# Optimization experiments

Measured on AMD Instinct MI355X. Metric: run time of the kernel, lower is better.

The kernel has to match this reference:

```python
import jax, jax.numpy as jnp
import numpy as np

CAPS = 16          # num_capsules
DIM = 16           # capsule_dim
NUM_ROUTING = 3
L2_EPS = 1e-12     # tf.nn.l2_normalize epsilon


def setup_inputs() -> dict:
    key = jax.random.key(0)
    k1, k2 = jax.random.split(key)
    inputs = jax.random.normal(k1, (16, 64, 64, 128), dtype=jnp.float32)
    # Conv2D kernel, HWIO layout, fan-in scaled like glorot-ish init
    kernel = jax.random.normal(k2, (3, 3, 128, CAPS * DIM), dtype=jnp.float32) * 0.03
    bias = jnp.zeros((CAPS * DIM,), dtype=jnp.float32)
    return {"inputs": inputs, "kernel": kernel, "bias": bias}


def reference(inputs, kernel, bias):
    # Conv2D(caps*dim, 3x3, padding='same', activation='relu'), channels_last
    x = jax.lax.conv_general_dilated(
        inputs, kernel, window_strides=(1, 1), padding="SAME",
        dimension_numbers=("NHWC", "HWIO", "NHWC"))
    x = jax.nn.relu(x + bias)
    B, H, W, _ = x.shape
    x = x.reshape(B, H * W, CAPS, DIM)            # (B, N, C, D)
    b = jnp.zeros((B, H * W, CAPS), dtype=x.dtype)
    v = None
    for _ in range(NUM_ROUTING):
        c = jax.nn.softmax(b, axis=-1)             # over capsules
        s = jnp.einsum("bnc,bncd->bcd", c, x)      # weighted sum over spatial
        # tf.nn.l2_normalize along last axis
        v = s * jax.lax.rsqrt(jnp.maximum(jnp.sum(s * s, axis=-1, keepdims=True), L2_EPS))
        b = b + jnp.einsum("bncd,bcd->bnc", x, v)  # agreement update
    # tile v over spatial dims: (B,1,1,C*D) -> (B,H,W,C*D)
    out = jnp.broadcast_to(v.reshape(B, 1, 1, CAPS * DIM), (B, H, W, CAPS * DIM))
    return out
```

## Files before the change

### kernel.cpp

```cpp
#include <hip/hip_runtime.h>
#include <hip/hip_bf16.h>

typedef unsigned short u16;
typedef unsigned int   u32;

typedef __bf16 bf16x8 __attribute__((ext_vector_type(8)));
typedef float  f32x4  __attribute__((ext_vector_type(4)));

#define GLDS(gp, lp) __builtin_amdgcn_global_load_lds( \
    (const __attribute__((address_space(1))) void*)(gp), \
    (__attribute__((address_space(3))) void*)(lp), 16, 0, 0)

__device__ __forceinline__ u16 f2b(float f) {
    __hip_bfloat16 h = __float2bfloat16(f);
    u16 u; __builtin_memcpy(&u, &h, 2); return u;
}
__device__ __forceinline__ float blo(u32 u) { return __uint_as_float(u << 16); }
__device__ __forceinline__ float bhi(u32 u) { return __uint_as_float(u & 0xffff0000u); }

__global__ void k_prep(const float* __restrict__ in, const float* __restrict__ wk,
                       u16* __restrict__ pad, u16* __restrict__ BF,
                       float* __restrict__ stats) {
    int bx = blockIdx.x, tid = threadIdx.x;
    if (bx < 4356) {
        int idx = bx * 256 + tid;
        int e0  = idx * 8;
        int ch  = e0 & 127;
        int rest = e0 >> 7;
        int pw = rest % 66;
        int r2 = rest / 66;
        int ph = r2 % 66;
        int b  = r2 / 66;
        u16 ov[8];
        if (ph >= 1 && ph <= 64 && pw >= 1 && pw <= 64) {
            const float* src = in + (((b * 64 + (ph - 1)) * 64 + (pw - 1)) * 128 + ch);
            const float4* s4 = (const float4*)src;
            float4 f0 = s4[0], f1 = s4[1];
            ov[0]=f2b(f0.x); ov[1]=f2b(f0.y); ov[2]=f2b(f0.z); ov[3]=f2b(f0.w);
            ov[4]=f2b(f1.x); ov[5]=f2b(f1.y); ov[6]=f2b(f1.z); ov[7]=f2b(f1.w);
        } else {
            #pragma unroll
            for (int j = 0; j < 8; ++j) ov[j] = 0;
        }
        uint4 w; __builtin_memcpy(&w, ov, 16);
        *(uint4*)(pad + e0) = w;
    } else if (bx < 5508) {
        int t = (bx - 4356) * 256 + tid;
        int j  = t & 7;
        int n  = (t >> 3) & 255;
        int q  = (t >> 11) & 3;
        int kk = (t >> 13) & 3;
        int p  = t >> 15;
        BF[t] = f2b(wk[(p * 128 + kk * 32 + q * 8 + j) * 256 + n]);
    } else {
        stats[(bx - 5508) * 256 + tid] = 0.f;
    }
}

__launch_bounds__(512, 2)
__global__ void k_conv(const u16* __restrict__ Ap, const u16* __restrict__ BF,
                       const float* __restrict__ bias,
                       u16* __restrict__ X, float* __restrict__ s0) {
    __shared__ u16 ldsA[25344];
    const int t = threadIdx.x;
    const int lane = t & 63, wid = t >> 6;
    const int q = lane >> 4, l15 = lane & 15;
    const int bb = blockIdx.x >> 4;
    const int rg = blockIdx.x & 15;
    const int rg4 = rg << 2;
    const int wm0 = (wid >> 2) << 7;
    const int wn0 = (wid & 3) << 6;
    const int rowb = wm0 >> 6;

#define STAGE(S) { \
    const int sb0 = wid * 396; \
    _Pragma("unroll") for (int i = 0; i < 6; ++i) { \
        int slot = sb0 + i * 64 + lane; \
        int pr = slot / 528; int rem = slot - pr * 528; \
        int wp = rem >> 3, cs = rem & 7; \
        int gc = (S) * 8 + (cs ^ (wp & 7)); \
        const u16* g = Ap + ((((bb * 66 + rg4 + pr) * 66 + wp) << 7) + (gc << 3)); \
        GLDS(g, (char*)ldsA + (sb0 + i * 64) * 16); \
    } \
    { int slot = sb0 + 384 + lane; \
      if (lane < 12) { \
        int pr = slot / 528; int rem = slot - pr * 528; \
        int wp = rem >> 3, cs = rem & 7; \
        int gc = (S) * 8 + (cs ^ (wp & 7)); \
        const u16* g = Ap + ((((bb * 66 + rg4 + pr) * 66 + wp) << 7) + (gc << 3)); \
        GLDS(g, (char*)ldsA + (sb0 + 384) * 16); \
      } } }

#define LOADB(B, P, S) { \
    _Pragma("unroll") for (int kk = 0; kk < 2; ++kk) \
    _Pragma("unroll") for (int ni = 0; ni < 4; ++ni) \
        B[kk * 4 + ni] = *(const bf16x8*)(BFl + (P) * 32768 + \
                                          ((S) * 2 + kk) * 8192 + ni * 128); }

#define COMPP(B, DH, DW) { \
    _Pragma("unroll") for (int kk = 0; kk < 2; ++kk) { \
        bf16x8 af[8]; \
        _Pragma("unroll") for (int mi = 0; mi < 8; ++mi) { \
            int wp = ((mi & 3) << 4) + l15 + (DW); \
            int pr = rowb + (mi >> 2) + (DH); \
            int cc = (kk << 2) + q; \
            af[mi] = *(const bf16x8*)((const char*)ldsA + \
                ((pr * 528 + (wp << 3) + (cc ^ (wp & 7))) << 4)); \
        } \
        _Pragma("unroll") for (int mi = 0; mi < 8; ++mi) \
        _Pragma("unroll") for (int ni = 0; ni < 4; ++ni) \
            acc[mi][ni] = __builtin_amdgcn_mfma_f32_16x16x32_bf16( \
                af[mi], B[kk * 4 + ni], acc[mi][ni], 0, 0, 0); } }

    const u16* BFl = BF + (q * 2048 + (wn0 + l15) * 8);

    f32x4 zero = {0.f, 0.f, 0.f, 0.f};
    f32x4 acc[8][4];
    #pragma unroll
    for (int mi = 0; mi < 8; ++mi)
        #pragma unroll
        for (int ni = 0; ni < 4; ++ni) acc[mi][ni] = zero;

    bf16x8 B0[8], B1[8];

    STAGE(0);
    __syncthreads();
    LOADB(B0, 0, 0);
    LOADB(B1, 1, 0); COMPP(B0, 0, 0);
    LOADB(B0, 2, 0); COMPP(B1, 0, 1);
    LOADB(B1, 3, 0); COMPP(B0, 0, 2);
    LOADB(B0, 4, 0); COMPP(B1, 1, 0);
    LOADB(B1, 5, 0); COMPP(B0, 1, 1);
    LOADB(B0, 6, 0); COMPP(B1, 1, 2);
    LOADB(B1, 7, 0); COMPP(B0, 2, 0);
    LOADB(B0, 8, 0); COMPP(B1, 2, 1);
    COMPP(B0, 2, 2);
    __syncthreads();

    STAGE(1);
    __syncthreads();
    LOADB(B0, 0, 1);
    LOADB(B1, 1, 1); COMPP(B0, 0, 0);
    LOADB(B0, 2, 1); COMPP(B1, 0, 1);
    LOADB(B1, 3, 1); COMPP(B0, 0, 2);
    LOADB(B0, 4, 1); COMPP(B1, 1, 0);
    LOADB(B1, 5, 1); COMPP(B0, 1, 1);
    LOADB(B0, 6, 1); COMPP(B1, 1, 2);
    LOADB(B1, 7, 1); COMPP(B0, 2, 0);
    LOADB(B0, 8, 1); COMPP(B1, 2, 1);
    COMPP(B0, 2, 2);

    float bv[4];
    #pragma unroll
    for (int ni = 0; ni < 4; ++ni) bv[ni] = bias[wn0 + ni * 16 + l15];
    float colsum[4] = {0.f, 0.f, 0.f, 0.f};
    u16* xrow = X + (((bb << 12) + (rg << 8) + wm0 + q * 4) * 256) + wn0 + l15;
    #pragma unroll
    for (int mi = 0; mi < 8; ++mi) {
        #pragma unroll
        for (int rr = 0; rr < 4; ++rr) {
            u16* xp = xrow + (mi * 16 + rr) * 256;
            #pragma unroll
            for (int ni = 0; ni < 4; ++ni) {
                float v = acc[mi][ni][rr] + bv[ni];
                v = v > 0.f ? v : 0.f;
                xp[ni * 16] = f2b(v);
                colsum[ni] += v;
            }
        }
    }
    #pragma unroll
    for (int ni = 0; ni < 4; ++ni) {
        float c = colsum[ni];
        c += __shfl_xor(c, 16);
        c += __shfl_xor(c, 32);
        if (lane < 16) atomicAdd(&s0[bb * 256 + wn0 + ni * 16 + l15], c);
    }
#undef STAGE
#undef LOADB
#undef COMPP
}

__global__ void k_pass(const u16* __restrict__ X, const float* __restrict__ Sa,
                       const float* __restrict__ Sb, float* __restrict__ Sout,
                       int use2) {
    __shared__ float v1s[256], v2s[256];
    __shared__ float red[4096];
    int t = threadIdx.x, b = blockIdx.y, chunk = blockIdx.x;
    {
        float sa = Sa[b * 256 + t];
        float ss = sa * sa;
        #pragma unroll
        for (int off = 1; off < 16; off <<= 1) ss += __shfl_xor(ss, off);
        ss = ss < 1e-12f ? 1e-12f : ss;
        v1s[t] = sa / sqrtf(ss);
        if (use2) {
            float sb = Sb[b * 256 + t];
            float s2 = sb * sb;
            #pragma unroll
            for (int off = 1; off < 16; off <<= 1) s2 += __shfl_xor(s2, off);
            s2 = s2 < 1e-12f ? 1e-12f : s2;
            v2s[t] = sb / sqrtf(s2);
        } else {
            v2s[t] = 0.f;
        }
    }
    __syncthreads();
    int c = t & 15, nl = t >> 4;
    float acc[16];
    #pragma unroll
    for (int d = 0; d < 16; ++d) acc[d] = 0.f;

    for (int r = 0; r < 8; ++r) {
        int n = chunk * 128 + r * 16 + nl;
        const u16* xp = X + ((b << 12) + n) * 256 + c * 16;
        uint4 a0 = ((const uint4*)xp)[0];
        uint4 a1 = ((const uint4*)xp)[1];
        u32 us[8] = {a0.x, a0.y, a0.z, a0.w, a1.x, a1.y, a1.z, a1.w};
        float xf[16];
        #pragma unroll
        for (int j = 0; j < 8; ++j) { xf[2*j] = blo(us[j]); xf[2*j+1] = bhi(us[j]); }
        float d1 = 0.f, d2 = 0.f;
        #pragma unroll
        for (int d = 0; d < 16; ++d) {
            d1 += xf[d] * v1s[c * 16 + d];
            d2 += xf[d] * v2s[c * 16 + d];
        }
        float bvv = use2 ? (d1 + d2) : d1;
        float mx = bvv;
        #pragma unroll
        for (int off = 1; off < 16; off <<= 1) {
            float o = __shfl_xor(mx, off);
            mx = mx > o ? mx : o;
        }
        float e = expf(bvv - mx);
        float sm = e;
        #pragma unroll
        for (int off = 1; off < 16; off <<= 1) sm += __shfl_xor(sm, off);
        float w = e / sm;
        #pragma unroll
        for (int d = 0; d < 16; ++d) acc[d] += w * xf[d];
    }
    #pragma unroll
    for (int d = 0; d < 16; ++d) red[t * 16 + d] = acc[d];
    __syncthreads();
    int c2 = t >> 4, d2i = t & 15;
    float tot = 0.f;
    #pragma unroll
    for (int n2 = 0; n2 < 16; ++n2) tot += red[(n2 * 16 + c2) * 16 + d2i];
    atomicAdd(&Sout[b * 256 + c2 * 16 + d2i], tot);
}

__global__ void k_bcast(const float* __restrict__ S, float* __restrict__ Out) {
    __shared__ float4 vls[64];
    int t = threadIdx.x, bx = blockIdx.x, b = blockIdx.y;
    float s = S[b * 256 + t];
    float ss = s * s;
    #pragma unroll
    for (int off = 1; off < 16; off <<= 1) ss += __shfl_xor(ss, off);
    ss = ss < 1e-12f ? 1e-12f : ss;
    ((float*)vls)[t] = s / sqrtf(ss);
    __syncthreads();
    float4* o = (float4*)Out + (long)b * 262144 + bx * 8192;
    #pragma unroll
    for (int j = 0; j < 32; ++j) {
        int idx = j * 256 + t;
        o[idx] = vls[idx & 63];
    }
}

extern "C" void kernel_launch(void* const* d_in, const int* in_sizes, int n_in,
                              void* d_out, int out_size, void* d_ws, size_t ws_size,
                              hipStream_t stream) {
    const float* in   = (const float*)d_in[0];
    const float* wk   = (const float*)d_in[1];
    const float* bias = (const float*)d_in[2];
    float* out = (float*)d_out;
    char* ws = (char*)d_ws;

    const size_t OFF_PAD = 0;
    const size_t OFF_BF  = 17842176;
    const size_t OFF_X   = 18432000;
    const size_t OFF_ST  = 51986432;
    const size_t NEEDED  = OFF_ST + 3 * 16384;
    if (ws_size < NEEDED) return;

    u16* pad = (u16*)(ws + OFF_PAD);
    u16* BF  = (u16*)(ws + OFF_BF);
    u16* X   = (u16*)(ws + OFF_X);
    float* s0 = (float*)(ws + OFF_ST);
    float* s2 = s0 + 4096;
    float* s3 = s2 + 4096;

    k_prep <<<5556, 256, 0, stream>>>(in, wk, pad, BF, s0);
    k_conv <<<256, 512, 0, stream>>>(pad, BF, bias, X, s0);
    k_pass <<<dim3(32, 16), 256, 0, stream>>>(X, s0, s0, s2, 0);
    k_pass <<<dim3(32, 16), 256, 0, stream>>>(X, s0, s2, s3, 1);
    k_bcast<<<dim3(32, 16), 256, 0, stream>>>(s3, out);
}
```

Measured before the change: 183.6 us.

## Shrink conv tiles to one output row per block and split routing passes finer

```diff
diff --git a/kernel.cpp b/kernel.cpp
--- a/kernel.cpp
+++ b/kernel.cpp
@@ -57,38 +57,37 @@
     }
 }
 
-__launch_bounds__(512, 2)
+__launch_bounds__(256, 2)
 __global__ void k_conv(const u16* __restrict__ Ap, const u16* __restrict__ BF,
                        const float* __restrict__ bias,
                        u16* __restrict__ X, float* __restrict__ s0) {
-    __shared__ u16 ldsA[25344];
+    __shared__ u16 ldsA[12672];
     const int t = threadIdx.x;
     const int lane = t & 63, wid = t >> 6;
     const int q = lane >> 4, l15 = lane & 15;
-    const int bb = blockIdx.x >> 4;
-    const int rg = blockIdx.x & 15;
-    const int rg4 = rg << 2;
-    const int wm0 = (wid >> 2) << 7;
-    const int wn0 = (wid & 3) << 6;
-    const int rowb = wm0 >> 6;
+    const int bb = blockIdx.x >> 6;
+    const int h  = blockIdx.x & 63;
+    const int wn0 = wid << 6;
 
 #define STAGE(S) { \
     const int sb0 = wid * 396; \
     _Pragma("unroll") for (int i = 0; i < 6; ++i) { \
-        int slot = sb0 + i * 64 + lane; \
+        int sb = sb0 + i * 64; \
+        int slot = sb + lane; \
         int pr = slot / 528; int rem = slot - pr * 528; \
         int wp = rem >> 3, cs = rem & 7; \
         int gc = (S) * 8 + (cs ^ (wp & 7)); \
-        const u16* g = Ap + ((((bb * 66 + rg4 + pr) * 66 + wp) << 7) + (gc << 3)); \
-        GLDS(g, (char*)ldsA + (sb0 + i * 64) * 16); \
+        const u16* g = Ap + ((((bb * 66 + h + pr) * 66 + wp) << 7) + (gc << 3)); \
+        GLDS(g, (char*)ldsA + sb * 16); \
     } \
-    { int slot = sb0 + 384 + lane; \
+    { int sb = sb0 + 384; \
       if (lane < 12) { \
+        int slot = sb + lane; \
         int pr = slot / 528; int rem = slot - pr * 528; \
         int wp = rem >> 3, cs = rem & 7; \
         int gc = (S) * 8 + (cs ^ (wp & 7)); \
-        const u16* g = Ap + ((((bb * 66 + rg4 + pr) * 66 + wp) << 7) + (gc << 3)); \
-        GLDS(g, (char*)ldsA + (sb0 + 384) * 16); \
+        const u16* g = Ap + ((((bb * 66 + h + pr) * 66 + wp) << 7) + (gc << 3)); \
+        GLDS(g, (char*)ldsA + sb * 16); \
       } } }
 
 #define LOADB(B, P, S) { \
@@ -99,15 +98,14 @@
 
 #define COMPP(B, DH, DW) { \
     _Pragma("unroll") for (int kk = 0; kk < 2; ++kk) { \
-        bf16x8 af[8]; \
-        _Pragma("unroll") for (int mi = 0; mi < 8; ++mi) { \
-            int wp = ((mi & 3) << 4) + l15 + (DW); \
-            int pr = rowb + (mi >> 2) + (DH); \
-            int cc = (kk << 2) + q; \
+        bf16x8 af[4]; \
+        _Pragma("unroll") for (int mi = 0; mi < 4; ++mi) { \
+            int wp = mi * 16 + l15 + (DW); \
+            int swz = (kk * 4 + q) ^ (wp & 7); \
             af[mi] = *(const bf16x8*)((const char*)ldsA + \
-                ((pr * 528 + (wp << 3) + (cc ^ (wp & 7))) << 4)); \
+                (((DH) * 528 + wp * 8 + swz) << 4)); \
         } \
-        _Pragma("unroll") for (int mi = 0; mi < 8; ++mi) \
+        _Pragma("unroll") for (int mi = 0; mi < 4; ++mi) \
         _Pragma("unroll") for (int ni = 0; ni < 4; ++ni) \
             acc[mi][ni] = __builtin_amdgcn_mfma_f32_16x16x32_bf16( \
                 af[mi], B[kk * 4 + ni], acc[mi][ni], 0, 0, 0); } }
@@ -115,9 +113,9 @@
     const u16* BFl = BF + (q * 2048 + (wn0 + l15) * 8);
 
     f32x4 zero = {0.f, 0.f, 0.f, 0.f};
-    f32x4 acc[8][4];
-    #pragma unroll
-    for (int mi = 0; mi < 8; ++mi)
+    f32x4 acc[4][4];
+    #pragma unroll
+    for (int mi = 0; mi < 4; ++mi)
         #pragma unroll
         for (int ni = 0; ni < 4; ++ni) acc[mi][ni] = zero;
 
@@ -154,9 +152,9 @@
     #pragma unroll
     for (int ni = 0; ni < 4; ++ni) bv[ni] = bias[wn0 + ni * 16 + l15];
     float colsum[4] = {0.f, 0.f, 0.f, 0.f};
-    u16* xrow = X + (((bb << 12) + (rg << 8) + wm0 + q * 4) * 256) + wn0 + l15;
-    #pragma unroll
-    for (int mi = 0; mi < 8; ++mi) {
+    u16* xrow = X + (((bb << 12) + (h << 6) + q * 4) * 256) + wn0 + l15;
+    #pragma unroll
+    for (int mi = 0; mi < 4; ++mi) {
         #pragma unroll
         for (int rr = 0; rr < 4; ++rr) {
             u16* xp = xrow + (mi * 16 + rr) * 256;
@@ -211,11 +209,16 @@
     #pragma unroll
     for (int d = 0; d < 16; ++d) acc[d] = 0.f;
 
-    for (int r = 0; r < 8; ++r) {
-        int n = chunk * 128 + r * 16 + nl;
-        const u16* xp = X + ((b << 12) + n) * 256 + c * 16;
-        uint4 a0 = ((const uint4*)xp)[0];
-        uint4 a1 = ((const uint4*)xp)[1];
+    const u16* xbase = X + ((b << 12) + chunk * 64 + nl) * 256 + c * 16;
+    uint4 p0 = ((const uint4*)xbase)[0];
+    uint4 p1 = ((const uint4*)xbase)[1];
+    for (int r = 0; r < 4; ++r) {
+        uint4 a0 = p0, a1 = p1;
+        if (r < 3) {
+            const u16* np = xbase + (r + 1) * 16 * 256;
+            p0 = ((const uint4*)np)[0];
+            p1 = ((const uint4*)np)[1];
+        }
         u32 us[8] = {a0.x, a0.y, a0.z, a0.w, a1.x, a1.y, a1.z, a1.w};
         float xf[16];
         #pragma unroll
@@ -227,13 +230,7 @@
             d2 += xf[d] * v2s[c * 16 + d];
         }
         float bvv = use2 ? (d1 + d2) : d1;
-        float mx = bvv;
-        #pragma unroll
-        for (int off = 1; off < 16; off <<= 1) {
-            float o = __shfl_xor(mx, off);
-            mx = mx > o ? mx : o;
-        }
-        float e = expf(bvv - mx);
+        float e = __expf(bvv);
         float sm = e;
         #pragma unroll
         for (int off = 1; off < 16; off <<= 1) sm += __shfl_xor(sm, off);
@@ -293,8 +290,8 @@
     float* s3 = s2 + 4096;
 
     k_prep <<<5556, 256, 0, stream>>>(in, wk, pad, BF, s0);
-    k_conv <<<256, 512, 0, stream>>>(pad, BF, bias, X, s0);
-    k_pass <<<dim3(32, 16), 256, 0, stream>>>(X, s0, s0, s2, 0);
-    k_pass <<<dim3(32, 16), 256, 0, stream>>>(X, s0, s2, s3, 1);
+    k_conv <<<1024, 256, 0, stream>>>(pad, BF, bias, X, s0);
+    k_pass <<<dim3(64, 16), 256, 0, stream>>>(X, s0, s0, s2, 0);
+    k_pass <<<dim3(64, 16), 256, 0, stream>>>(X, s0, s2, s3, 1);
     k_bcast<<<dim3(32, 16), 256, 0, stream>>>(s3, out);
 }
```

New measurement: 163.5 us. 1.12x faster.
